# Kernel tuning notes

Hardware: AMD Instinct MI355X
Metric: run time of the kernel (lower is better)

The kernel has to match this reference:

```python
import jax, jax.numpy as jnp
import numpy as np

N_NODES = 100000
N_EDGES = 1000000
N_GRAPHS = 16
CUTOFF = 6.0
ETAS = [0.5, 1.0, 2.0, 4.0]
OFFSETS = [0.0, 1.0, 2.0, 3.0, 4.0, 5.0, 6.0, 7.0]
SPECIES = (0, 1, 2)


def setup_inputs() -> dict:
    key = jax.random.key(0)
    ks = jax.random.split(key, 6)
    pos = jax.random.normal(ks[0], (N_NODES, 3), dtype=jnp.float32)
    cell = jax.random.normal(ks[1], (N_GRAPHS, 3, 3), dtype=jnp.float32)
    edge_shift = jax.random.normal(ks[2], (N_EDGES, 3), dtype=jnp.float32)
    z = jax.random.randint(ks[3], (N_NODES,), 0, 3, dtype=jnp.int64)
    edge_index = jax.random.randint(ks[4], (2, N_EDGES), 0, N_NODES, dtype=jnp.int64)
    batch = jnp.sort(jax.random.randint(ks[5], (N_NODES,), 0, N_GRAPHS, dtype=jnp.int64))
    # buffers from torch.cartesian_prod(etas, offsets).t(): etas repeated, offsets tiled
    etas = jnp.repeat(jnp.asarray(ETAS, dtype=jnp.float32), len(OFFSETS))      # [P]
    offsets = jnp.tile(jnp.asarray(OFFSETS, dtype=jnp.float32), len(ETAS))     # [P]
    return {"pos": pos, "cell": cell, "edge_shift": edge_shift, "etas": etas,
            "offsets": offsets, "z": z, "edge_index": edge_index, "batch": batch}


def reference(pos, cell, edge_shift, etas, offsets, z, edge_index, batch):
    i = edge_index[0]  # receiver
    j = edge_index[1]  # sender
    # periodic-image-shifted edge vectors: [E,3]
    vec_ij = pos[j] - pos[i] + jnp.einsum('ni,nij->nj', edge_shift, cell[batch[i]])
    r_ij = jnp.linalg.norm(vec_ij, axis=-1)  # [E]
    # cosine cutoff
    fc = jnp.where(r_ij < CUTOFF, 0.5 * (jnp.cos(jnp.pi * r_ij / CUTOFF) + 1.0), 0.0)
    # Gaussian RBF per (eta, offset) pair: [P, E]
    G2_ij = jnp.exp(-etas[:, None] * (r_ij - offsets[:, None]) ** 2 / CUTOFF ** 2) * fc
    zj = z[j]
    outs = []
    for sp in SPECIES:  # small fixed loop over species (3)
        m = (zj == sp).astype(G2_ij.dtype)          # [E]
        seg = jax.ops.segment_sum((G2_ij * m).T, i, num_segments=pos.shape[0])  # [N, P]
        outs.append(seg.T)                           # [P, N]
    return jnp.concatenate(outs, axis=0)             # [S*P, N]
```

## Files before the change

### kernel.cpp

```cpp
#include <hip/hip_runtime.h>
#include <math.h>

#define N_NODES 100000
#define N_EDGES 1000000
#define NPAIR 32
#define CUTOFF 6.0f

#define CHUNK 128
#define NCHUNK ((N_NODES + CHUNK - 1) / CHUNK)
#define CAP 2048
#define K1_BLOCKS 256
#define K1_THREADS 1024
#define EPB ((N_EDGES + K1_BLOCKS - 1) / K1_BLOCKS)

__global__ __launch_bounds__(1024) void bin_kernel(
    const float* __restrict__ pos,
    const float* __restrict__ cell,
    const float* __restrict__ shift,
    const int*   __restrict__ z,
    const int*   __restrict__ ei,
    const int*   __restrict__ batch,
    unsigned int* __restrict__ bucket,
    int*          __restrict__ cur)
{
    __shared__ int lhist[NCHUNK];
    __shared__ int lbase[NCHUNK];
    int tid = threadIdx.x;

    for (int c = tid; c < NCHUNK; c += K1_THREADS) lhist[c] = 0;
    __syncthreads();

    int base = blockIdx.x * EPB;
    int lim  = min(base + EPB, N_EDGES);

    unsigned int recs[4];
    int chks[4];
    int locs[4];

#pragma unroll
    for (int q = 0; q < 4; ++q) {
        chks[q] = -1;
        int e = base + tid + q * K1_THREADS;
        if (e < lim) {
            int i = ei[e];
            int j = ei[N_EDGES + e];
            float sx = shift[3 * e + 0];
            float sy = shift[3 * e + 1];
            float sz = shift[3 * e + 2];
            const float* C = cell + 9 * batch[i];
            float vx = pos[3 * j + 0] - pos[3 * i + 0] + sx * C[0] + sy * C[3] + sz * C[6];
            float vy = pos[3 * j + 1] - pos[3 * i + 1] + sx * C[1] + sy * C[4] + sz * C[7];
            float vz = pos[3 * j + 2] - pos[3 * i + 2] + sx * C[2] + sy * C[5] + sz * C[8];
            float r = sqrtf(vx * vx + vy * vy + vz * vz);
            if (r < CUTOFF) {
                unsigned int qq = (unsigned int)(r * (8388608.0f / 6.0f));
                qq = min(qq, 8388607u);
                int c = i >> 7;
                recs[q] = (qq << 9) | ((unsigned int)(i & 127) << 2) | (unsigned int)(z[j] & 3);
                chks[q] = c;
                locs[q] = atomicAdd(&lhist[c], 1);
            }
        }
    }
    __syncthreads();

    for (int c = tid; c < NCHUNK; c += K1_THREADS) {
        int h = lhist[c];
        lbase[c] = (h > 0) ? atomicAdd(&cur[c * 16], h) : 0;
    }
    __syncthreads();

#pragma unroll
    for (int q = 0; q < 4; ++q) {
        if (chks[q] >= 0) {
            int slot = lbase[chks[q]] + locs[q];
            if (slot < CAP)
                bucket[(size_t)chks[q] * CAP + slot] = recs[q];
        }
    }
}

__global__ __launch_bounds__(128) void sortaccum_kernel(
    const unsigned int* __restrict__ bucket,
    const int*          __restrict__ cur,
    float*              __restrict__ out)
{
    __shared__ unsigned int sorted[CAP];
    __shared__ int lhist[CHUNK];
    __shared__ int lcur[CHUNK];
    int tid = threadIdx.x;
    int chunk = blockIdx.x;

    lhist[tid] = 0;
    __syncthreads();

    int cnt = min(cur[chunk * 16], CAP);
    const unsigned int* b = bucket + (size_t)chunk * CAP;

    unsigned int regs[16];
#pragma unroll
    for (int it = 0; it < 16; ++it) {
        int k = tid + it * 128;
        unsigned int rc = 0xFFFFFFFFu;
        if (k < cnt) {
            rc = b[k];
            atomicAdd(&lhist[(rc >> 2) & 127], 1);
        }
        regs[it] = rc;
    }
    __syncthreads();

    int c0 = lhist[tid];
    for (int d = 1; d < 128; d <<= 1) {
        int y = (tid >= d) ? lhist[tid - d] : 0;
        __syncthreads();
        lhist[tid] += y;
        __syncthreads();
    }
    int incl = lhist[tid];
    int s_beg = incl - c0;
    lcur[tid] = s_beg;
    __syncthreads();

#pragma unroll
    for (int it = 0; it < 16; ++it) {
        unsigned int rc = regs[it];
        if (rc != 0xFFFFFFFFu) {
            int slot = atomicAdd(&lcur[(rc >> 2) & 127], 1);
            sorted[slot] = rc;
        }
    }
    __syncthreads();

    float a0[NPAIR], a1[NPAIR], a2[NPAIR];
#pragma unroll
    for (int p = 0; p < NPAIR; ++p) { a0[p] = 0.0f; a1[p] = 0.0f; a2[p] = 0.0f; }

    for (int k = s_beg; k < incl; ++k) {
        unsigned int rc = sorted[k];
        int spec = rc & 3;
        float r = (float)(rc >> 9) * (6.0f / 8388608.0f);
        float fc = 0.5f * (__cosf(r * (float)(M_PI / 6.0)) + 1.0f);
        float m0 = (spec == 0) ? fc : 0.0f;
        float m1 = (spec == 1) ? fc : 0.0f;
        float m2 = (spec == 2) ? fc : 0.0f;
#pragma unroll
        for (int o = 0; o < 8; ++o) {
            float d = r - (float)o;
            float e0 = __expf(d * d * (-0.5f / 36.0f));
            float e1 = e0 * e0;
            float e2 = e1 * e1;
            float e3 = e2 * e2;
            a0[o]      = fmaf(m0, e0, a0[o]);
            a1[o]      = fmaf(m1, e0, a1[o]);
            a2[o]      = fmaf(m2, e0, a2[o]);
            a0[8 + o]  = fmaf(m0, e1, a0[8 + o]);
            a1[8 + o]  = fmaf(m1, e1, a1[8 + o]);
            a2[8 + o]  = fmaf(m2, e1, a2[8 + o]);
            a0[16 + o] = fmaf(m0, e2, a0[16 + o]);
            a1[16 + o] = fmaf(m1, e2, a1[16 + o]);
            a2[16 + o] = fmaf(m2, e2, a2[16 + o]);
            a0[24 + o] = fmaf(m0, e3, a0[24 + o]);
            a1[24 + o] = fmaf(m1, e3, a1[24 + o]);
            a2[24 + o] = fmaf(m2, e3, a2[24 + o]);
        }
    }

    int node = chunk * CHUNK + tid;
    if (node < N_NODES) {
#pragma unroll
        for (int p = 0; p < NPAIR; ++p) {
            out[(size_t)(0 * NPAIR + p) * N_NODES + node] = a0[p];
            out[(size_t)(1 * NPAIR + p) * N_NODES + node] = a1[p];
            out[(size_t)(2 * NPAIR + p) * N_NODES + node] = a2[p];
        }
    }
}

extern "C" void kernel_launch(void* const* d_in, const int* in_sizes, int n_in,
                              void* d_out, int out_size, void* d_ws, size_t ws_size,
                              hipStream_t stream) {
    const float* pos   = (const float*)d_in[0];
    const float* cell  = (const float*)d_in[1];
    const float* shift = (const float*)d_in[2];
    const int*   z     = (const int*)d_in[5];
    const int*   ei    = (const int*)d_in[6];
    const int*   batch = (const int*)d_in[7];
    float* out = (float*)d_out;

    char* ws = (char*)d_ws;
    unsigned int* bucket = (unsigned int*)(ws);
    int*          cur    = (int*)(ws + (size_t)NCHUNK * CAP * 4);

    hipMemsetAsync(cur, 0, NCHUNK * 16 * sizeof(int), stream);

    bin_kernel<<<K1_BLOCKS, K1_THREADS, 0, stream>>>(pos, cell, shift, z, ei, batch,
                                                     bucket, cur);
    sortaccum_kernel<<<NCHUNK, 128, 0, stream>>>(bucket, cur, out);
}
```

Before: 64.39 us.

## Split each node's edge accumulation across two threads and double binning blocks

The sort-accumulate kernel now runs 256 threads per chunk, with two threads per node taking alternating edges, combining partial sums by lane shuffle, and splitting the output stores between them. The binning kernel launches twice as many blocks with two edges per thread instead of four. Both changes aim to raise parallelism and occupancy and to shorten the serial per-node loop. The cost is extra shuffle reductions over 96 accumulators per thread and more global atomics on the chunk counters.

```diff
diff --git a/kernel.cpp b/kernel.cpp
--- a/kernel.cpp
+++ b/kernel.cpp
@@ -9,9 +9,10 @@
 #define CHUNK 128
 #define NCHUNK ((N_NODES + CHUNK - 1) / CHUNK)
 #define CAP 2048
-#define K1_BLOCKS 256
+#define K1_BLOCKS 512
 #define K1_THREADS 1024
 #define EPB ((N_EDGES + K1_BLOCKS - 1) / K1_BLOCKS)
+#define ST 256
 
 __global__ __launch_bounds__(1024) void bin_kernel(
     const float* __restrict__ pos,
@@ -27,18 +28,18 @@
     __shared__ int lbase[NCHUNK];
     int tid = threadIdx.x;
 
-    for (int c = tid; c < NCHUNK; c += K1_THREADS) lhist[c] = 0;
+    if (tid < NCHUNK) lhist[tid] = 0;
     __syncthreads();
 
     int base = blockIdx.x * EPB;
     int lim  = min(base + EPB, N_EDGES);
 
-    unsigned int recs[4];
-    int chks[4];
-    int locs[4];
-
-#pragma unroll
-    for (int q = 0; q < 4; ++q) {
+    unsigned int recs[2];
+    int chks[2];
+    int locs[2];
+
+#pragma unroll
+    for (int q = 0; q < 2; ++q) {
         chks[q] = -1;
         int e = base + tid + q * K1_THREADS;
         if (e < lim) {
@@ -64,14 +65,14 @@
     }
     __syncthreads();
 
-    for (int c = tid; c < NCHUNK; c += K1_THREADS) {
-        int h = lhist[c];
-        lbase[c] = (h > 0) ? atomicAdd(&cur[c * 16], h) : 0;
-    }
-    __syncthreads();
-
-#pragma unroll
-    for (int q = 0; q < 4; ++q) {
+    if (tid < NCHUNK) {
+        int h = lhist[tid];
+        lbase[tid] = (h > 0) ? atomicAdd(&cur[tid * 16], h) : 0;
+    }
+    __syncthreads();
+
+#pragma unroll
+    for (int q = 0; q < 2; ++q) {
         if (chks[q] >= 0) {
             int slot = lbase[chks[q]] + locs[q];
             if (slot < CAP)
@@ -80,7 +81,7 @@
     }
 }
 
-__global__ __launch_bounds__(128) void sortaccum_kernel(
+__global__ __launch_bounds__(ST) void sortaccum_kernel(
     const unsigned int* __restrict__ bucket,
     const int*          __restrict__ cur,
     float*              __restrict__ out)
@@ -91,16 +92,16 @@
     int tid = threadIdx.x;
     int chunk = blockIdx.x;
 
-    lhist[tid] = 0;
+    if (tid < CHUNK) lhist[tid] = 0;
     __syncthreads();
 
     int cnt = min(cur[chunk * 16], CAP);
     const unsigned int* b = bucket + (size_t)chunk * CAP;
 
-    unsigned int regs[16];
-#pragma unroll
-    for (int it = 0; it < 16; ++it) {
-        int k = tid + it * 128;
+    unsigned int regs[CAP / ST];
+#pragma unroll
+    for (int it = 0; it < CAP / ST; ++it) {
+        int k = tid + it * ST;
         unsigned int rc = 0xFFFFFFFFu;
         if (k < cnt) {
             rc = b[k];
@@ -110,20 +111,23 @@
     }
     __syncthreads();
 
-    int c0 = lhist[tid];
-    for (int d = 1; d < 128; d <<= 1) {
-        int y = (tid >= d) ? lhist[tid - d] : 0;
+    for (int d = 1; d < CHUNK; d <<= 1) {
+        int y = 0;
+        if (tid < CHUNK && tid >= d) y = lhist[tid - d];
         __syncthreads();
-        lhist[tid] += y;
+        if (tid < CHUNK) lhist[tid] += y;
         __syncthreads();
     }
-    int incl = lhist[tid];
-    int s_beg = incl - c0;
-    lcur[tid] = s_beg;
-    __syncthreads();
-
-#pragma unroll
-    for (int it = 0; it < 16; ++it) {
+    if (tid < CHUNK) {
+        int incl = lhist[tid];
+        int c0 = (tid > 0) ? lhist[tid - 1] : 0;
+        lcur[tid] = c0;
+        (void)incl;
+    }
+    __syncthreads();
+
+#pragma unroll
+    for (int it = 0; it < CAP / ST; ++it) {
         unsigned int rc = regs[it];
         if (rc != 0xFFFFFFFFu) {
             int slot = atomicAdd(&lcur[(rc >> 2) & 127], 1);
@@ -132,11 +136,16 @@
     }
     __syncthreads();
 
+    int node_loc = tid >> 1;
+    int par = tid & 1;
+    int s_beg = (node_loc > 0) ? lhist[node_loc - 1] : 0;
+    int incl = lhist[node_loc];
+
     float a0[NPAIR], a1[NPAIR], a2[NPAIR];
 #pragma unroll
     for (int p = 0; p < NPAIR; ++p) { a0[p] = 0.0f; a1[p] = 0.0f; a2[p] = 0.0f; }
 
-    for (int k = s_beg; k < incl; ++k) {
+    for (int k = s_beg + par; k < incl; k += 2) {
         unsigned int rc = sorted[k];
         int spec = rc & 3;
         float r = (float)(rc >> 9) * (6.0f / 8388608.0f);
@@ -166,13 +175,29 @@
         }
     }
 
-    int node = chunk * CHUNK + tid;
+#pragma unroll
+    for (int p = 0; p < NPAIR; ++p) {
+        a0[p] += __shfl_xor(a0[p], 1);
+        a1[p] += __shfl_xor(a1[p], 1);
+        a2[p] += __shfl_xor(a2[p], 1);
+    }
+
+    int node = chunk * CHUNK + node_loc;
     if (node < N_NODES) {
-#pragma unroll
-        for (int p = 0; p < NPAIR; ++p) {
-            out[(size_t)(0 * NPAIR + p) * N_NODES + node] = a0[p];
-            out[(size_t)(1 * NPAIR + p) * N_NODES + node] = a1[p];
-            out[(size_t)(2 * NPAIR + p) * N_NODES + node] = a2[p];
+        if (par == 0) {
+#pragma unroll
+            for (int p = 0; p < NPAIR; ++p)
+                out[(size_t)p * N_NODES + node] = a0[p];
+#pragma unroll
+            for (int p = 0; p < 16; ++p)
+                out[(size_t)(NPAIR + p) * N_NODES + node] = a1[p];
+        } else {
+#pragma unroll
+            for (int p = 16; p < NPAIR; ++p)
+                out[(size_t)(NPAIR + p) * N_NODES + node] = a1[p];
+#pragma unroll
+            for (int p = 0; p < NPAIR; ++p)
+                out[(size_t)(2 * NPAIR + p) * N_NODES + node] = a2[p];
         }
     }
 }
@@ -196,5 +221,5 @@
 
     bin_kernel<<<K1_BLOCKS, K1_THREADS, 0, stream>>>(pos, cell, shift, z, ei, batch,
                                                      bucket, cur);
-    sortaccum_kernel<<<NCHUNK, 128, 0, stream>>>(bucket, cur, out);
+    sortaccum_kernel<<<NCHUNK, ST, 0, stream>>>(bucket, cur, out);
 }
```

Measured after the change: 71.18 us. 10.5% more time.

## Widen node chunks, batch gather loads, pad bucket reservations to 16

Applied to the files above, without the earlier changes.

Node chunks grow from 128 to 512 nodes, so there are fewer buckets and the accumulate kernel runs 512 threads per block with an 8192-entry capacity. The radius quantization drops to 21 bits to make room for the wider local index. The bin kernel now uses a fixed 4 edges per thread, which changes the block count, and issues all index, shift and position gathers up front to raise memory-level parallelism. Each block's bucket reservation is rounded up to a multiple of 16 and the padding is filled with sentinel records that the accumulate kernel filters out, so bucket writes are more aligned. The cost is more sentinel writes, lower radius precision, a larger shared-memory footprint, and an overflow risk if a chunk exceeds 8192 entries.

```diff
diff --git a/kernel.cpp b/kernel.cpp
--- a/kernel.cpp
+++ b/kernel.cpp
@@ -6,12 +6,14 @@
 #define NPAIR 32
 #define CUTOFF 6.0f
 
-#define CHUNK 128
+#define CHUNK 512
 #define NCHUNK ((N_NODES + CHUNK - 1) / CHUNK)
-#define CAP 2048
-#define K1_BLOCKS 256
+#define CAP 8192
 #define K1_THREADS 1024
-#define EPB ((N_EDGES + K1_BLOCKS - 1) / K1_BLOCKS)
+#define EPT 4
+#define EPB (K1_THREADS * EPT)
+#define K1_BLOCKS ((N_EDGES + EPB - 1) / EPB)
+#define AT 512
 
 __global__ __launch_bounds__(1024) void bin_kernel(
     const float* __restrict__ pos,
@@ -27,36 +29,53 @@
     __shared__ int lbase[NCHUNK];
     int tid = threadIdx.x;
 
-    for (int c = tid; c < NCHUNK; c += K1_THREADS) lhist[c] = 0;
+    if (tid < NCHUNK) lhist[tid] = 0;
     __syncthreads();
 
     int base = blockIdx.x * EPB;
-    int lim  = min(base + EPB, N_EDGES);
-
-    unsigned int recs[4];
-    int chks[4];
-    int locs[4];
-
-#pragma unroll
-    for (int q = 0; q < 4; ++q) {
+
+    int iv[EPT], jv[EPT];
+    float sx[EPT], sy[EPT], sz[EPT];
+    bool val[EPT];
+#pragma unroll
+    for (int q = 0; q < EPT; ++q) {
+        int e = base + tid + q * K1_THREADS;
+        val[q] = (e < N_EDGES);
+        int ee = val[q] ? e : 0;
+        iv[q] = ei[ee];
+        jv[q] = ei[N_EDGES + ee];
+        sx[q] = shift[3 * ee + 0];
+        sy[q] = shift[3 * ee + 1];
+        sz[q] = shift[3 * ee + 2];
+    }
+
+    float pix[EPT], piy[EPT], piz[EPT], pjx[EPT], pjy[EPT], pjz[EPT];
+    int zj[EPT], bi[EPT];
+#pragma unroll
+    for (int q = 0; q < EPT; ++q) {
+        pix[q] = pos[3 * iv[q] + 0]; piy[q] = pos[3 * iv[q] + 1]; piz[q] = pos[3 * iv[q] + 2];
+        pjx[q] = pos[3 * jv[q] + 0]; pjy[q] = pos[3 * jv[q] + 1]; pjz[q] = pos[3 * jv[q] + 2];
+        zj[q] = z[jv[q]];
+        bi[q] = batch[iv[q]];
+    }
+
+    unsigned int recs[EPT];
+    int chks[EPT], locs[EPT];
+#pragma unroll
+    for (int q = 0; q < EPT; ++q) {
         chks[q] = -1;
-        int e = base + tid + q * K1_THREADS;
-        if (e < lim) {
-            int i = ei[e];
-            int j = ei[N_EDGES + e];
-            float sx = shift[3 * e + 0];
-            float sy = shift[3 * e + 1];
-            float sz = shift[3 * e + 2];
-            const float* C = cell + 9 * batch[i];
-            float vx = pos[3 * j + 0] - pos[3 * i + 0] + sx * C[0] + sy * C[3] + sz * C[6];
-            float vy = pos[3 * j + 1] - pos[3 * i + 1] + sx * C[1] + sy * C[4] + sz * C[7];
-            float vz = pos[3 * j + 2] - pos[3 * i + 2] + sx * C[2] + sy * C[5] + sz * C[8];
+        if (val[q]) {
+            const float* C = cell + 9 * bi[q];
+            float vx = pjx[q] - pix[q] + sx[q] * C[0] + sy[q] * C[3] + sz[q] * C[6];
+            float vy = pjy[q] - piy[q] + sx[q] * C[1] + sy[q] * C[4] + sz[q] * C[7];
+            float vz = pjz[q] - piz[q] + sx[q] * C[2] + sy[q] * C[5] + sz[q] * C[8];
             float r = sqrtf(vx * vx + vy * vy + vz * vz);
             if (r < CUTOFF) {
-                unsigned int qq = (unsigned int)(r * (8388608.0f / 6.0f));
-                qq = min(qq, 8388607u);
-                int c = i >> 7;
-                recs[q] = (qq << 9) | ((unsigned int)(i & 127) << 2) | (unsigned int)(z[j] & 3);
+                unsigned int qq = (unsigned int)(r * (2097152.0f / 6.0f));
+                qq = min(qq, 2097151u);
+                int c = iv[q] >> 9;
+                recs[q] = (qq << 11) | ((unsigned int)(iv[q] & 511) << 2)
+                        | (unsigned int)(zj[q] & 3);
                 chks[q] = c;
                 locs[q] = atomicAdd(&lhist[c], 1);
             }
@@ -64,69 +83,80 @@
     }
     __syncthreads();
 
-    for (int c = tid; c < NCHUNK; c += K1_THREADS) {
-        int h = lhist[c];
-        lbase[c] = (h > 0) ? atomicAdd(&cur[c * 16], h) : 0;
-    }
-    __syncthreads();
-
-#pragma unroll
-    for (int q = 0; q < 4; ++q) {
+    if (tid < NCHUNK) {
+        int h  = lhist[tid];
+        int hp = (h + 15) & ~15;
+        lbase[tid] = (hp > 0) ? atomicAdd(&cur[tid * 16], hp) : 0;
+    }
+    __syncthreads();
+
+#pragma unroll
+    for (int q = 0; q < EPT; ++q) {
         if (chks[q] >= 0) {
             int slot = lbase[chks[q]] + locs[q];
             if (slot < CAP)
                 bucket[(size_t)chks[q] * CAP + slot] = recs[q];
         }
     }
+
+    if (tid < NCHUNK) {
+        int h  = lhist[tid];
+        int hp = (h + 15) & ~15;
+        int b  = lbase[tid];
+        for (int k = h; k < hp; ++k) {
+            int slot = b + k;
+            if (slot < CAP)
+                bucket[(size_t)tid * CAP + slot] = 0xFFFFFFFFu;
+        }
+    }
 }
 
-__global__ __launch_bounds__(128) void sortaccum_kernel(
+__global__ __launch_bounds__(AT) void accum_kernel(
     const unsigned int* __restrict__ bucket,
     const int*          __restrict__ cur,
     float*              __restrict__ out)
 {
     __shared__ unsigned int sorted[CAP];
-    __shared__ int lhist[CHUNK];
+    __shared__ int hist[CHUNK];
     __shared__ int lcur[CHUNK];
     int tid = threadIdx.x;
     int chunk = blockIdx.x;
 
-    lhist[tid] = 0;
+    hist[tid] = 0;
     __syncthreads();
 
     int cnt = min(cur[chunk * 16], CAP);
     const unsigned int* b = bucket + (size_t)chunk * CAP;
 
-    unsigned int regs[16];
-#pragma unroll
-    for (int it = 0; it < 16; ++it) {
-        int k = tid + it * 128;
+    unsigned int regs[CAP / AT];
+#pragma unroll
+    for (int it = 0; it < CAP / AT; ++it) {
+        int k = tid + it * AT;
         unsigned int rc = 0xFFFFFFFFu;
-        if (k < cnt) {
-            rc = b[k];
-            atomicAdd(&lhist[(rc >> 2) & 127], 1);
-        }
+        if (k < cnt) rc = b[k];
+        if ((rc & 3u) == 3u) rc = 0xFFFFFFFFu;
+        else atomicAdd(&hist[(rc >> 2) & 511], 1);
         regs[it] = rc;
     }
     __syncthreads();
 
-    int c0 = lhist[tid];
-    for (int d = 1; d < 128; d <<= 1) {
-        int y = (tid >= d) ? lhist[tid - d] : 0;
+    int c0 = hist[tid];
+    for (int d = 1; d < CHUNK; d <<= 1) {
+        int y = (tid >= d) ? hist[tid - d] : 0;
         __syncthreads();
-        lhist[tid] += y;
+        hist[tid] += y;
         __syncthreads();
     }
-    int incl = lhist[tid];
-    int s_beg = incl - c0;
-    lcur[tid] = s_beg;
-    __syncthreads();
-
-#pragma unroll
-    for (int it = 0; it < 16; ++it) {
+    int incl = hist[tid];
+    int beg  = incl - c0;
+    lcur[tid] = beg;
+    __syncthreads();
+
+#pragma unroll
+    for (int it = 0; it < CAP / AT; ++it) {
         unsigned int rc = regs[it];
         if (rc != 0xFFFFFFFFu) {
-            int slot = atomicAdd(&lcur[(rc >> 2) & 127], 1);
+            int slot = atomicAdd(&lcur[(rc >> 2) & 511], 1);
             sorted[slot] = rc;
         }
     }
@@ -136,10 +166,10 @@
 #pragma unroll
     for (int p = 0; p < NPAIR; ++p) { a0[p] = 0.0f; a1[p] = 0.0f; a2[p] = 0.0f; }
 
-    for (int k = s_beg; k < incl; ++k) {
+    for (int k = beg; k < incl; ++k) {
         unsigned int rc = sorted[k];
         int spec = rc & 3;
-        float r = (float)(rc >> 9) * (6.0f / 8388608.0f);
+        float r = (float)(rc >> 11) * (6.0f / 2097152.0f);
         float fc = 0.5f * (__cosf(r * (float)(M_PI / 6.0)) + 1.0f);
         float m0 = (spec == 0) ? fc : 0.0f;
         float m1 = (spec == 1) ? fc : 0.0f;
@@ -196,5 +226,5 @@
 
     bin_kernel<<<K1_BLOCKS, K1_THREADS, 0, stream>>>(pos, cell, shift, z, ei, batch,
                                                      bucket, cur);
-    sortaccum_kernel<<<NCHUNK, 128, 0, stream>>>(bucket, cur, out);
+    accum_kernel<<<NCHUNK, AT, 0, stream>>>(bucket, cur, out);
 }
```

Result: no change. 63.40 us (-1.5%).
